# Performance work log

Measured on AMD Instinct MI355X. Metric: run time of the kernel, lower is better.

Reference implementation:

```python
import jax, jax.numpy as jnp
import numpy as np

B, S, D_IN, D_OUT = 4, 2048, 2048, 2048
E, R = 8, 8
SCALING = 16.0 / 8.0  # lora_alpha / r
# Dropout (p=0.05) treated as identity (eval mode) for a deterministic reference.

def setup_inputs() -> dict:
    key = jax.random.key(0)
    ks = jax.random.split(key, 8)
    x = jax.random.normal(ks[0], (B, S, D_IN), dtype=jnp.float32)
    base_W = jax.random.normal(ks[1], (D_OUT, D_IN), dtype=jnp.float32) * 0.02
    base_b = jax.random.normal(ks[2], (D_OUT,), dtype=jnp.float32) * 0.02
    shared_A = jax.random.normal(ks[3], (R, D_IN), dtype=jnp.float32) * 0.01
    shared_B = jax.random.normal(ks[4], (D_OUT, R), dtype=jnp.float32) * 0.01
    expert_A = jax.random.normal(ks[5], (E, R, D_IN), dtype=jnp.float32) * 0.01
    expert_B = jax.random.normal(ks[6], (E, D_OUT, R), dtype=jnp.float32) * 0.01
    task_emb = jax.random.normal(ks[7], (E, D_IN), dtype=jnp.float32) * 0.01
    collab_w = jnp.array(0.5, dtype=jnp.float32)
    return {"x": x, "base_W": base_W, "base_b": base_b,
            "shared_A": shared_A, "shared_B": shared_B,
            "expert_A": expert_A, "expert_B": expert_B,
            "task_emb": task_emb, "collab_w": collab_w}

def reference(x, base_W, base_b, shared_A, shared_B, expert_A, expert_B, task_emb, collab_w):
    # base linear: [B,S,D_out]
    base_out = jnp.einsum('bsi,oi->bso', x, base_W) + base_b
    # shared LoRA path
    shared_out = jnp.einsum('bsr,or->bso', jnp.einsum('bsi,ri->bsr', x, shared_A), shared_B) * SCALING
    # soft routing over task experts (task_id=None branch)
    x_mean = x.mean(axis=1)                               # [B,D_in]
    routing = jax.nn.softmax(x_mean @ task_emb.T, axis=-1)  # [B,E]
    t = jnp.einsum('bsi,eri->bser', x, expert_A)          # [B,S,E,R] low-rank
    task_out = jnp.einsum('bser,eor,be->bso', t, expert_B, routing) * SCALING
    cw = jax.nn.sigmoid(collab_w)
    return base_out + cw * shared_out + (1.0 - cw) * task_out
```

## Files before the change

kernel.cpp:

```cpp
#include <hip/hip_runtime.h>
#include <hip/hip_bf16.h>
#include <math.h>

#define BATCH 4
#define SEQ   2048
#define DIN   2048
#define DOUT  2048
#define NEXP  8
#define RANK  8
#define MTOT  (BATCH * SEQ)
#define KE    64
#define NKC   8

typedef __bf16 bf16x8 __attribute__((ext_vector_type(8)));
typedef __bf16 bf16x4 __attribute__((ext_vector_type(4)));
typedef float  f32x4  __attribute__((ext_vector_type(4)));

#define GLOBAL_AS __attribute__((address_space(1)))
#define LDS_AS    __attribute__((address_space(3)))

#define BARRIER() asm volatile("s_barrier" ::: "memory")

__global__ __launch_bounds__(256) void mega_prep(
    const float* __restrict__ x, const float* __restrict__ W,
    const float* __restrict__ expert_A, const float* __restrict__ shared_A,
    const float* __restrict__ expert_B, const float* __restrict__ shared_B,
    const float* __restrict__ task_emb, const float* __restrict__ collab,
    __bf16* __restrict__ xb, __bf16* __restrict__ Wb,
    __bf16* __restrict__ caug, __bf16* __restrict__ pt, float* __restrict__ plog)
{
    const int bid = blockIdx.x;
    const int t = threadIdx.x;

    if (bid >= 512) {
        if (bid < 4608) {
            size_t idx = ((size_t)(bid - 512) * 256 + t) * 4;
            int o = (int)(idx >> 11), i = (int)(idx & 2047);
            float cw = 1.0f / (1.0f + expf(-collab[0]));
            float s = cw * 2.0f;
            float4 w = *(const float4*)&W[idx];
            float dx = 0.f, dy = 0.f, dz = 0.f, dw = 0.f;
            #pragma unroll
            for (int r = 0; r < 8; ++r) {
                float bs = shared_B[(size_t)o * RANK + r];
                float4 as = *(const float4*)&shared_A[(size_t)r * DIN + i];
                dx += bs * as.x; dy += bs * as.y; dz += bs * as.z; dw += bs * as.w;
            }
            bf16x4 h = { (__bf16)(w.x + s * dx), (__bf16)(w.y + s * dy),
                         (__bf16)(w.z + s * dz), (__bf16)(w.w + s * dw) };
            *(bf16x4*)&Wb[idx] = h;
        } else {
            int idx = ((bid - 4608) * 256 + t) * 4;
            int o = idx >> 6, k = idx & 63;
            float cw = 1.0f / (1.0f + expf(-collab[0]));
            float s = (1.0f - cw) * 2.0f;
            float4 v = *(const float4*)&expert_B[((size_t)(k >> 3) * DOUT + o) * RANK + (k & 7)];
            bf16x4 h = { (__bf16)(s * v.x), (__bf16)(s * v.y),
                         (__bf16)(s * v.z), (__bf16)(s * v.w) };
            *(bf16x4*)&caug[idx] = h;
        }
        return;
    }

    __shared__ __bf16 lsA[128 * 64];
    __shared__ __bf16 lsB[96 * 64];
    __shared__ float lsc[32];
    const int lane = t & 63;
    const int w = t >> 6;
    const int kc = bid & 7;
    const int m0 = (bid >> 3) * 128;

    f32x4 acc[2][5];
    #pragma unroll
    for (int a = 0; a < 2; ++a)
        #pragma unroll
        for (int c = 0; c < 5; ++c) acc[a][c] = (f32x4){0.f, 0.f, 0.f, 0.f};

    for (int it = 0; it < 4; ++it) {
        int k0 = kc * 256 + it * 64;
        #pragma unroll
        for (int q = 0; q < 4; ++q) {
            int row = q * 32 + (t >> 3), sl = t & 7, seg = sl ^ (row & 7);
            const float* gp = x + (size_t)(m0 + row) * DIN + k0 + seg * 8;
            float4 v0 = *(const float4*)gp;
            float4 v1 = *(const float4*)(gp + 4);
            bf16x8 h = { (__bf16)v0.x, (__bf16)v0.y, (__bf16)v0.z, (__bf16)v0.w,
                         (__bf16)v1.x, (__bf16)v1.y, (__bf16)v1.z, (__bf16)v1.w };
            *(bf16x8*)&lsA[row * 64 + sl * 8] = h;
            *(bf16x8*)&xb[(size_t)(m0 + row) * DIN + k0 + seg * 8] = h;
        }
        #pragma unroll
        for (int q = 0; q < 3; ++q) {
            int c = q * 256 + t;
            int row = c >> 3, sl = c & 7, seg = sl ^ (row & 7);
            bf16x8 h = { (__bf16)0.f, (__bf16)0.f, (__bf16)0.f, (__bf16)0.f,
                         (__bf16)0.f, (__bf16)0.f, (__bf16)0.f, (__bf16)0.f };
            if (row < 64) {
                const float* gp = expert_A + (size_t)row * DIN + k0 + seg * 8;
                float4 v0 = *(const float4*)gp, v1 = *(const float4*)(gp + 4);
                h = bf16x8{ (__bf16)v0.x, (__bf16)v0.y, (__bf16)v0.z, (__bf16)v0.w,
                            (__bf16)v1.x, (__bf16)v1.y, (__bf16)v1.z, (__bf16)v1.w };
            } else if (row < 72) {
                const float* gp = task_emb + (size_t)(row - 64) * DIN + k0 + seg * 8;
                float4 v0 = *(const float4*)gp, v1 = *(const float4*)(gp + 4);
                h = bf16x8{ (__bf16)v0.x, (__bf16)v0.y, (__bf16)v0.z, (__bf16)v0.w,
                            (__bf16)v1.x, (__bf16)v1.y, (__bf16)v1.z, (__bf16)v1.w };
            }
            *(bf16x8*)&lsB[row * 64 + sl * 8] = h;
        }
        __syncthreads();
        #pragma unroll
        for (int kk = 0; kk < 2; ++kk) {
            bf16x8 af[2], bfr[5];
            #pragma unroll
            for (int tm = 0; tm < 2; ++tm) {
                int r = w * 32 + tm * 16 + (lane & 15);
                int slot = (kk * 4 + (lane >> 4)) ^ (r & 7);
                af[tm] = *(const bf16x8*)&lsA[r * 64 + slot * 8];
            }
            #pragma unroll
            for (int tn = 0; tn < 5; ++tn) {
                int r = tn * 16 + (lane & 15);
                int slot = (kk * 4 + (lane >> 4)) ^ (r & 7);
                bfr[tn] = *(const bf16x8*)&lsB[r * 64 + slot * 8];
            }
            #pragma unroll
            for (int tm = 0; tm < 2; ++tm)
                #pragma unroll
                for (int tn = 0; tn < 5; ++tn)
                    acc[tm][tn] = __builtin_amdgcn_mfma_f32_16x16x32_bf16(
                        af[tm], bfr[tn], acc[tm][tn], 0, 0, 0);
        }
        __syncthreads();
    }

    #pragma unroll
    for (int tm = 0; tm < 2; ++tm)
        #pragma unroll
        for (int tn = 0; tn < 4; ++tn) {
            int col = tn * 16 + (lane & 15);
            #pragma unroll
            for (int v = 0; v < 4; ++v) {
                int row = m0 + w * 32 + tm * 16 + (lane >> 4) * 4 + v;
                pt[((size_t)kc * MTOT + row) * KE + col] = (__bf16)acc[tm][tn][v];
            }
        }

    float s = 0.f;
    #pragma unroll
    for (int tm = 0; tm < 2; ++tm)
        #pragma unroll
        for (int v = 0; v < 4; ++v) s += acc[tm][4][v];
    s += __shfl_down(s, 32);
    s += __shfl_down(s, 16);
    if (lane < 8) lsc[w * 8 + lane] = s;
    __syncthreads();
    if (t < 8)
        plog[bid * 8 + t] = lsc[t] + lsc[8 + t] + lsc[16 + t] + lsc[24 + t];
}

__global__ __launch_bounds__(512, 2) void gemm_main(
    const __bf16* __restrict__ xb, const __bf16* __restrict__ Wb,
    const __bf16* __restrict__ pt, const __bf16* __restrict__ caug,
    const float* __restrict__ plog, const float* __restrict__ bias,
    float* __restrict__ out)
{
    __shared__ __bf16 lds[65536];
    const int t = threadIdx.x;
    const int lane = t & 63;
    const int wid = t >> 6;
    const int wm = wid >> 2, wn = wid & 3;
    const int bid = blockIdx.x;
    const int xcd = bid & 7, j = bid >> 3;
    const int m0 = (xcd * 4 + (j >> 3)) * 256;
    const int n0 = (j & 7) * 256;
    const int b  = m0 >> 11;

    const int srow = t >> 3;
    const int sseg = (t & 7) ^ (srow & 7);
    const __bf16* gA = xb + (size_t)(m0 + srow) * DIN + sseg * 8;
    const __bf16* gB = Wb + (size_t)(n0 + srow) * DIN + sseg * 8;
    const int lbase = (t & ~63) * 8;

    int aoff[8], boff[4];
    #pragma unroll
    for (int fm = 0; fm < 8; ++fm) {
        int r = wm * 128 + fm * 16 + (lane & 15);
        aoff[fm] = r * 64 + (((lane >> 4) ^ (r & 7)) * 8);
    }
    #pragma unroll
    for (int fn = 0; fn < 4; ++fn) {
        int r = wn * 64 + fn * 16 + (lane & 15);
        boff[fn] = r * 64 + (((lane >> 4) ^ (r & 7)) * 8);
    }

    f32x4 acc[8][4];
    #pragma unroll
    for (int i = 0; i < 8; ++i)
        #pragma unroll
        for (int jj = 0; jj < 4; ++jj) acc[i][jj] = (f32x4){0.f, 0.f, 0.f, 0.f};

    #pragma unroll
    for (int q = 0; q < 4; ++q) {
        __builtin_amdgcn_global_load_lds((GLOBAL_AS void*)(gA + q * 64 * DIN),
            (LDS_AS void*)&lds[q * 4096 + lbase], 16, 0, 0);
        __builtin_amdgcn_global_load_lds((GLOBAL_AS void*)(gB + q * 64 * DIN),
            (LDS_AS void*)&lds[32768 + q * 4096 + lbase], 16, 0, 0);
    }
    asm volatile("s_waitcnt vmcnt(0)" ::: "memory");
    BARRIER();

    for (int kt = 0; kt < 32; ++kt) {
        const int abase = (kt & 1) * 16384;
        const int bbase = 32768 + (kt & 1) * 16384;
        if (kt < 31) {
            const int nb = ((kt & 1) ^ 1) * 16384;
            const __bf16* a2 = gA + (kt + 1) * 64;
            const __bf16* b2 = gB + (kt + 1) * 64;
            #pragma unroll
            for (int q = 0; q < 4; ++q) {
                __builtin_amdgcn_global_load_lds((GLOBAL_AS void*)(a2 + q * 64 * DIN),
                    (LDS_AS void*)&lds[nb + q * 4096 + lbase], 16, 0, 0);
                __builtin_amdgcn_global_load_lds((GLOBAL_AS void*)(b2 + q * 64 * DIN),
                    (LDS_AS void*)&lds[32768 + nb + q * 4096 + lbase], 16, 0, 0);
            }
        }
        bf16x8 bfrag[4][2];
        #pragma unroll
        for (int fn = 0; fn < 4; ++fn) {
            bfrag[fn][0] = *(const bf16x8*)&lds[bbase + boff[fn]];
            bfrag[fn][1] = *(const bf16x8*)&lds[bbase + (boff[fn] ^ 32)];
        }
        #pragma unroll
        for (int p = 0; p < 4; ++p) {
            bf16x8 afr[2][2];
            #pragma unroll
            for (int i = 0; i < 2; ++i) {
                int fm = p * 2 + i;
                afr[i][0] = *(const bf16x8*)&lds[abase + aoff[fm]];
                afr[i][1] = *(const bf16x8*)&lds[abase + (aoff[fm] ^ 32)];
            }
            BARRIER();
            __builtin_amdgcn_s_setprio(1);
            #pragma unroll
            for (int kk = 0; kk < 2; ++kk)
                #pragma unroll
                for (int i = 0; i < 2; ++i)
                    #pragma unroll
                    for (int fn = 0; fn < 4; ++fn)
                        acc[p * 2 + i][fn] = __builtin_amdgcn_mfma_f32_16x16x32_bf16(
                            afr[i][kk], bfrag[fn][kk], acc[p * 2 + i][fn], 0, 0, 0);
            __builtin_amdgcn_s_setprio(0);
            if (p == 3 && kt < 31)
                asm volatile("s_waitcnt vmcnt(0)" ::: "memory");
            BARRIER();
        }
    }

    {
        const __bf16* gC = caug + (size_t)(n0 + srow) * KE + sseg * 8;
        #pragma unroll
        for (int q = 0; q < 4; ++q)
            __builtin_amdgcn_global_load_lds((GLOBAL_AS void*)(gC + q * 64 * KE),
                (LDS_AS void*)&lds[32768 + q * 4096 + lbase], 16, 0, 0);
    }
    float* scr = (float*)&lds[16384];
    float* lgs = scr + 512;
    {
        const float* pb = plog + (size_t)b * 128 * 8;
        int e = t & 7, rr = t >> 3;
        scr[rr * 8 + e] = pb[rr * 8 + e] + pb[(rr + 64) * 8 + e];
    }
    asm volatile("s_waitcnt lgkmcnt(0)" ::: "memory");
    BARRIER();
    if (t < 8) {
        float s = 0.f;
        #pragma unroll
        for (int i = 0; i < 64; ++i) s += scr[i * 8 + t];
        lgs[t] = s;
    }
    asm volatile("s_waitcnt lgkmcnt(0)" ::: "memory");
    BARRIER();
    float f[NEXP];
    {
        float li[NEXP];
        #pragma unroll
        for (int e = 0; e < NEXP; ++e) li[e] = lgs[e] * (1.0f / (float)SEQ);
        float mx = li[0];
        #pragma unroll
        for (int e = 1; e < NEXP; ++e) mx = fmaxf(mx, li[e]);
        float den = 0.f;
        #pragma unroll
        for (int e = 0; e < NEXP; ++e) { f[e] = expf(li[e] - mx); den += f[e]; }
        float rden = 1.0f / den;
        #pragma unroll
        for (int e = 0; e < NEXP; ++e) f[e] *= rden;
    }
    #pragma unroll
    for (int q = 0; q < 4; ++q) {
        int row = q * 64 + srow;
        const __bf16* p0 = pt + (size_t)(m0 + row) * KE + sseg * 8;
        float sum[8] = {0.f, 0.f, 0.f, 0.f, 0.f, 0.f, 0.f, 0.f};
        #pragma unroll
        for (int kc = 0; kc < NKC; ++kc) {
            bf16x8 v = *(const bf16x8*)(p0 + (size_t)kc * MTOT * KE);
            #pragma unroll
            for (int jj = 0; jj < 8; ++jj) sum[jj] += (float)v[jj];
        }
        float fe = f[sseg];
        bf16x8 h;
        #pragma unroll
        for (int jj = 0; jj < 8; ++jj) h[jj] = (__bf16)(sum[jj] * fe);
        *(bf16x8*)&lds[row * 64 + (t & 7) * 8] = h;
    }
    asm volatile("s_waitcnt vmcnt(0) lgkmcnt(0)" ::: "memory");
    BARRIER();
    {
        bf16x8 bfrag[4][2];
        #pragma unroll
        for (int fn = 0; fn < 4; ++fn) {
            bfrag[fn][0] = *(const bf16x8*)&lds[32768 + boff[fn]];
            bfrag[fn][1] = *(const bf16x8*)&lds[32768 + (boff[fn] ^ 32)];
        }
        #pragma unroll
        for (int fm = 0; fm < 8; ++fm) {
            bf16x8 a0 = *(const bf16x8*)&lds[aoff[fm]];
            bf16x8 a1 = *(const bf16x8*)&lds[aoff[fm] ^ 32];
            #pragma unroll
            for (int fn = 0; fn < 4; ++fn) {
                acc[fm][fn] = __builtin_amdgcn_mfma_f32_16x16x32_bf16(
                    a0, bfrag[fn][0], acc[fm][fn], 0, 0, 0);
                acc[fm][fn] = __builtin_amdgcn_mfma_f32_16x16x32_bf16(
                    a1, bfrag[fn][1], acc[fm][fn], 0, 0, 0);
            }
        }
    }

    #pragma unroll
    for (int fn = 0; fn < 4; ++fn) {
        int col = n0 + wn * 64 + fn * 16 + (lane & 15);
        float bv = bias[col];
        #pragma unroll
        for (int fm = 0; fm < 8; ++fm) {
            int row = m0 + wm * 128 + fm * 16 + (lane >> 4) * 4;
            #pragma unroll
            for (int v = 0; v < 4; ++v)
                out[(size_t)(row + v) * DOUT + col] = acc[fm][fn][v] + bv;
        }
    }
}

extern "C" void kernel_launch(void* const* d_in, const int* in_sizes, int n_in,
                              void* d_out, int out_size, void* d_ws, size_t ws_size,
                              hipStream_t stream)
{
    const float* x        = (const float*)d_in[0];
    const float* base_W   = (const float*)d_in[1];
    const float* base_b   = (const float*)d_in[2];
    const float* shared_A = (const float*)d_in[3];
    const float* shared_B = (const float*)d_in[4];
    const float* expert_A = (const float*)d_in[5];
    const float* expert_B = (const float*)d_in[6];
    const float* task_emb = (const float*)d_in[7];
    const float* collab_w = (const float*)d_in[8];
    float* out = (float*)d_out;

    char* ws = (char*)d_ws;
    __bf16* xb   = (__bf16*)(ws + 0);
    __bf16* Wb   = (__bf16*)(ws + 33554432);
    __bf16* pt   = (__bf16*)(ws + 41943040);
    __bf16* caug = (__bf16*)(ws + 50331648);
    float*  plog = (float*) (ws + 50593792);

    mega_prep<<<dim3(4736), 256, 0, stream>>>(x, base_W, expert_A, shared_A,
                                              expert_B, shared_B, task_emb, collab_w,
                                              xb, Wb, caug, pt, plog);
    gemm_main<<<dim3(256), 512, 0, stream>>>(xb, Wb, pt, caug, plog, base_b, out);
}
```

Before: 234.0 us.

## Prefetch two K-tiles ahead with split load groups and partial vmcnt waits

Restructures the main GEMM loop so global-to-LDS loads for tile kt+2 (B plus half of A) and the rest of A for kt+1 are issued at different phases of the inner loop. It waits with vmcnt(8) instead of vmcnt(0), keeping several loads in flight across iterations. The aim is to hide global memory latency that the one-tile-ahead prefetch with a full drain left exposed. The buffer-reuse timing across the double buffer is subtle, and a mistake in the wait counts could race.

Measured after the change: 231.9 us. Within noise of the previous version (-0.9%).

```diff
diff --git a/kernel.cpp b/kernel.cpp
--- a/kernel.cpp
+++ b/kernel.cpp
@@ -158,6 +158,33 @@
     if (t < 8)
         plog[bid * 8 + t] = lsc[t] + lsc[8 + t] + lsc[16 + t] + lsc[24 + t];
 }
+
+#define ISSUE_G1(j) do {                                                      \
+    const int nb_ = ((j) & 1) * 16384;                                        \
+    const __bf16* a_ = gA + (j) * 64;                                         \
+    const __bf16* b_ = gB + (j) * 64;                                         \
+    __builtin_amdgcn_global_load_lds((GLOBAL_AS void*)(b_ + 0 * 64 * DIN),    \
+        (LDS_AS void*)&lds[32768 + nb_ + 0 * 4096 + lbase], 16, 0, 0);        \
+    __builtin_amdgcn_global_load_lds((GLOBAL_AS void*)(b_ + 1 * 64 * DIN),    \
+        (LDS_AS void*)&lds[32768 + nb_ + 1 * 4096 + lbase], 16, 0, 0);        \
+    __builtin_amdgcn_global_load_lds((GLOBAL_AS void*)(b_ + 2 * 64 * DIN),    \
+        (LDS_AS void*)&lds[32768 + nb_ + 2 * 4096 + lbase], 16, 0, 0);        \
+    __builtin_amdgcn_global_load_lds((GLOBAL_AS void*)(b_ + 3 * 64 * DIN),    \
+        (LDS_AS void*)&lds[32768 + nb_ + 3 * 4096 + lbase], 16, 0, 0);        \
+    __builtin_amdgcn_global_load_lds((GLOBAL_AS void*)(a_ + 0 * 64 * DIN),    \
+        (LDS_AS void*)&lds[nb_ + 0 * 4096 + lbase], 16, 0, 0);                \
+    __builtin_amdgcn_global_load_lds((GLOBAL_AS void*)(a_ + 2 * 64 * DIN),    \
+        (LDS_AS void*)&lds[nb_ + 2 * 4096 + lbase], 16, 0, 0);                \
+} while (0)
+
+#define ISSUE_G2(j) do {                                                      \
+    const int nb_ = ((j) & 1) * 16384;                                        \
+    const __bf16* a_ = gA + (j) * 64;                                         \
+    __builtin_amdgcn_global_load_lds((GLOBAL_AS void*)(a_ + 1 * 64 * DIN),    \
+        (LDS_AS void*)&lds[nb_ + 1 * 4096 + lbase], 16, 0, 0);                \
+    __builtin_amdgcn_global_load_lds((GLOBAL_AS void*)(a_ + 3 * 64 * DIN),    \
+        (LDS_AS void*)&lds[nb_ + 3 * 4096 + lbase], 16, 0, 0);                \
+} while (0)
 
 __global__ __launch_bounds__(512, 2) void gemm_main(
     const __bf16* __restrict__ xb, const __bf16* __restrict__ Wb,
@@ -200,61 +227,98 @@
         #pragma unroll
         for (int jj = 0; jj < 4; ++jj) acc[i][jj] = (f32x4){0.f, 0.f, 0.f, 0.f};
 
-    #pragma unroll
-    for (int q = 0; q < 4; ++q) {
-        __builtin_amdgcn_global_load_lds((GLOBAL_AS void*)(gA + q * 64 * DIN),
-            (LDS_AS void*)&lds[q * 4096 + lbase], 16, 0, 0);
-        __builtin_amdgcn_global_load_lds((GLOBAL_AS void*)(gB + q * 64 * DIN),
-            (LDS_AS void*)&lds[32768 + q * 4096 + lbase], 16, 0, 0);
-    }
-    asm volatile("s_waitcnt vmcnt(0)" ::: "memory");
+    ISSUE_G1(0); ISSUE_G2(0); ISSUE_G1(1);
+    asm volatile("s_waitcnt vmcnt(8)" ::: "memory");
     BARRIER();
 
     for (int kt = 0; kt < 32; ++kt) {
         const int abase = (kt & 1) * 16384;
         const int bbase = 32768 + (kt & 1) * 16384;
-        if (kt < 31) {
-            const int nb = ((kt & 1) ^ 1) * 16384;
-            const __bf16* a2 = gA + (kt + 1) * 64;
-            const __bf16* b2 = gB + (kt + 1) * 64;
-            #pragma unroll
-            for (int q = 0; q < 4; ++q) {
-                __builtin_amdgcn_global_load_lds((GLOBAL_AS void*)(a2 + q * 64 * DIN),
-                    (LDS_AS void*)&lds[nb + q * 4096 + lbase], 16, 0, 0);
-                __builtin_amdgcn_global_load_lds((GLOBAL_AS void*)(b2 + q * 64 * DIN),
-                    (LDS_AS void*)&lds[32768 + nb + q * 4096 + lbase], 16, 0, 0);
-            }
-        }
         bf16x8 bfrag[4][2];
+        bf16x8 afr[2][2];
+
+        if (kt < 31) ISSUE_G2(kt + 1);
         #pragma unroll
         for (int fn = 0; fn < 4; ++fn) {
             bfrag[fn][0] = *(const bf16x8*)&lds[bbase + boff[fn]];
             bfrag[fn][1] = *(const bf16x8*)&lds[bbase + (boff[fn] ^ 32)];
         }
         #pragma unroll
-        for (int p = 0; p < 4; ++p) {
-            bf16x8 afr[2][2];
-            #pragma unroll
-            for (int i = 0; i < 2; ++i) {
-                int fm = p * 2 + i;
-                afr[i][0] = *(const bf16x8*)&lds[abase + aoff[fm]];
-                afr[i][1] = *(const bf16x8*)&lds[abase + (aoff[fm] ^ 32)];
-            }
-            BARRIER();
-            __builtin_amdgcn_s_setprio(1);
-            #pragma unroll
-            for (int kk = 0; kk < 2; ++kk)
+        for (int i = 0; i < 2; ++i) {
+            afr[i][0] = *(const bf16x8*)&lds[abase + aoff[i]];
+            afr[i][1] = *(const bf16x8*)&lds[abase + (aoff[i] ^ 32)];
+        }
+        BARRIER();
+        __builtin_amdgcn_s_setprio(1);
+        #pragma unroll
+        for (int kk = 0; kk < 2; ++kk)
+            #pragma unroll
+            for (int i = 0; i < 2; ++i)
                 #pragma unroll
-                for (int i = 0; i < 2; ++i)
-                    #pragma unroll
-                    for (int fn = 0; fn < 4; ++fn)
-                        acc[p * 2 + i][fn] = __builtin_amdgcn_mfma_f32_16x16x32_bf16(
-                            afr[i][kk], bfrag[fn][kk], acc[p * 2 + i][fn], 0, 0, 0);
-            __builtin_amdgcn_s_setprio(0);
-            if (p == 3 && kt < 31)
-                asm volatile("s_waitcnt vmcnt(0)" ::: "memory");
-            BARRIER();
-        }
+                for (int fn = 0; fn < 4; ++fn)
+                    acc[i][fn] = __builtin_amdgcn_mfma_f32_16x16x32_bf16(
+                        afr[i][kk], bfrag[fn][kk], acc[i][fn], 0, 0, 0);
+        __builtin_amdgcn_s_setprio(0);
+        BARRIER();
+
+        #pragma unroll
+        for (int i = 0; i < 2; ++i) {
+            afr[i][0] = *(const bf16x8*)&lds[abase + aoff[2 + i]];
+            afr[i][1] = *(const bf16x8*)&lds[abase + (aoff[2 + i] ^ 32)];
+        }
+        BARRIER();
+        __builtin_amdgcn_s_setprio(1);
+        #pragma unroll
+        for (int kk = 0; kk < 2; ++kk)
+            #pragma unroll
+            for (int i = 0; i < 2; ++i)
+                #pragma unroll
+                for (int fn = 0; fn < 4; ++fn)
+                    acc[2 + i][fn] = __builtin_amdgcn_mfma_f32_16x16x32_bf16(
+                        afr[i][kk], bfrag[fn][kk], acc[2 + i][fn], 0, 0, 0);
+        __builtin_amdgcn_s_setprio(0);
+        if (kt < 31) asm volatile("s_waitcnt vmcnt(8)" ::: "memory");
+        else         asm volatile("s_waitcnt vmcnt(0)" ::: "memory");
+        BARRIER();
+
+        if (kt < 30) ISSUE_G1(kt + 2);
+        #pragma unroll
+        for (int i = 0; i < 2; ++i) {
+            afr[i][0] = *(const bf16x8*)&lds[abase + aoff[4 + i]];
+            afr[i][1] = *(const bf16x8*)&lds[abase + (aoff[4 + i] ^ 32)];
+        }
+        BARRIER();
+        __builtin_amdgcn_s_setprio(1);
+        #pragma unroll
+        for (int kk = 0; kk < 2; ++kk)
+            #pragma unroll
+            for (int i = 0; i < 2; ++i)
+                #pragma unroll
+                for (int fn = 0; fn < 4; ++fn)
+                    acc[4 + i][fn] = __builtin_amdgcn_mfma_f32_16x16x32_bf16(
+                        afr[i][kk], bfrag[fn][kk], acc[4 + i][fn], 0, 0, 0);
+        __builtin_amdgcn_s_setprio(0);
+        BARRIER();
+
+        #pragma unroll
+        for (int i = 0; i < 2; ++i) {
+            afr[i][0] = *(const bf16x8*)&lds[abase + aoff[6 + i]];
+            afr[i][1] = *(const bf16x8*)&lds[abase + (aoff[6 + i] ^ 32)];
+        }
+        BARRIER();
+        __builtin_amdgcn_s_setprio(1);
+        #pragma unroll
+        for (int kk = 0; kk < 2; ++kk)
+            #pragma unroll
+            for (int i = 0; i < 2; ++i)
+                #pragma unroll
+                for (int fn = 0; fn < 4; ++fn)
+                    acc[6 + i][fn] = __builtin_amdgcn_mfma_f32_16x16x32_bf16(
+                        afr[i][kk], bfrag[fn][kk], acc[6 + i][fn], 0, 0, 0);
+        __builtin_amdgcn_s_setprio(0);
+        if (kt < 30)       asm volatile("s_waitcnt vmcnt(8)" ::: "memory");
+        else if (kt == 30) asm volatile("s_waitcnt vmcnt(2)" ::: "memory");
+        BARRIER();
     }
 
     {
```
